# Optimization experiments

Measured on AMD Instinct MI355X. Metric: run time of the kernel, lower is better.

## Reference

```python
import jax, jax.numpy as jnp
import numpy as np

D_MODEL = 512
N_HEADS = 8
D_K = D_MODEL // N_HEADS
WINDOW = 32  # attention restricted to |i-j| <= WINDOW//2
SCALE = float(np.sqrt(D_K))


def setup_inputs() -> dict:
    key = jax.random.key(0)
    ks = jax.random.split(key, 11)
    B, S, D = 2, 4096, D_MODEL
    inv = 1.0 / np.sqrt(D)
    inp = {
        "query": jax.random.normal(ks[0], (B, S, D), jnp.float32),
        "key": jax.random.normal(ks[1], (B, S, D), jnp.float32),
        "value": jax.random.normal(ks[2], (B, S, D), jnp.float32),
        # torch nn.Linear params: weight (out,in), bias (out,)
        "wq": jax.random.uniform(ks[3], (D, D), jnp.float32, -inv, inv),
        "bq": jax.random.uniform(ks[4], (D,), jnp.float32, -inv, inv),
        "wk": jax.random.uniform(ks[5], (D, D), jnp.float32, -inv, inv),
        "bk": jax.random.uniform(ks[6], (D,), jnp.float32, -inv, inv),
        "wv": jax.random.uniform(ks[7], (D, D), jnp.float32, -inv, inv),
        "bv": jax.random.uniform(ks[8], (D,), jnp.float32, -inv, inv),
        "wo": jax.random.uniform(ks[9], (D, D), jnp.float32, -inv, inv),
        "bo": jax.random.uniform(ks[10], (D,), jnp.float32, -inv, inv),
    }
    return inp


def _linear(x, w, b):
    # torch: y = x @ w.T + b
    return jnp.einsum('bsd,od->bso', x, w) + b


def reference(query, key, value, wq, bq, wk, bk, wv, bv, wo, bo):
    B, S, D = query.shape
    # project and split heads -> [B, H, S, d_k]
    def split(x):
        return x.reshape(B, S, N_HEADS, D_K).transpose(0, 2, 1, 3)
    Q = split(_linear(query, wq, bq))
    K = split(_linear(key, wk, bk))
    V = split(_linear(value, wv, bv))
    # full scores then banded mask (faithful to original dense-masked impl)
    scores = jnp.einsum('bhqd,bhkd->bhqk', Q, K) / SCALE
    i = jnp.arange(S)[:, None]
    j = jnp.arange(S)[None, :]
    band = jnp.abs(i - j) <= (WINDOW // 2)  # [S, S]
    scores = jnp.where(band[None, None, :, :], scores, -1e9)
    attn = jax.nn.softmax(scores, axis=-1)
    ctx = jnp.einsum('bhqk,bhkd->bhqd', attn, V)
    ctx = ctx.transpose(0, 2, 1, 3).reshape(B, S, D)
    return _linear(ctx, wo, bo)
```

## Files before the change

kernel.cpp:

```cpp
#include <hip/hip_runtime.h>
#include <hip/hip_bf16.h>

using u16 = unsigned short;
using u32 = unsigned int;

typedef float f32x4 __attribute__((ext_vector_type(4)));
typedef __bf16 bf16x8 __attribute__((ext_vector_type(8)));

constexpr int B_ = 2;
constexpr int S_ = 4096;
constexpr int D_ = 512;
constexpr int H_ = 8;
constexpr int DK_ = 64;
constexpr int M_ = B_ * S_;
constexpr int K_ = 512;

__device__ __forceinline__ float bf2f(u16 u) {
  return __uint_as_float(((u32)u) << 16);
}
__device__ __forceinline__ u16 f2bf(float x) {
  u32 u = __float_as_uint(x);
  u = (u + 0x7fffu + ((u >> 16) & 1u)) >> 16;
  return (u16)u;
}
__device__ __forceinline__ u32 pack2(float a, float b) {
  return (u32)f2bf(a) | ((u32)f2bf(b) << 16);
}
__device__ __forceinline__ u32 cvtpk(float a, float b) {
  u32 r;
  asm("v_cvt_pk_bf16_f32 %0, %1, %2" : "=v"(r) : "v"(a), "v"(b));
  return r;
}

__device__ __forceinline__ void gload16(const void* g, void* l) {
  __builtin_amdgcn_global_load_lds((const __attribute__((address_space(1))) void*)g,
                                   (__attribute__((address_space(3))) void*)l,
                                   16, 0, 0);
}

constexpr int NG_W = 4 * (262144 / 8);

__global__ __launch_bounds__(256) void convert_w(
    const float* __restrict__ wq, const float* __restrict__ wk,
    const float* __restrict__ wv, const float* __restrict__ wo,
    u16* __restrict__ wqb, u16* __restrict__ wkb, u16* __restrict__ wvb,
    u16* __restrict__ wob)
{
  const int g8 = blockIdx.x * 256 + threadIdx.x;
  if (g8 >= NG_W) return;
  const int t = g8 >> 15;
  const int r = g8 & 32767;
  const float* s = (t == 0) ? wq : (t == 1) ? wk : (t == 2) ? wv : wo;
  u16* d = (t == 0) ? wqb : (t == 1) ? wkb : (t == 2) ? wvb : wob;
  const size_t off = (size_t)r * 8;
  const float4 x = *(const float4*)(s + off);
  const float4 y = *(const float4*)(s + off + 4);
  uint4 o;
  o.x = pack2(x.x, x.y); o.y = pack2(x.z, x.w);
  o.z = pack2(y.x, y.y); o.w = pack2(y.z, y.w);
  *(uint4*)(d + off) = o;
}

template<int MODE>
__device__ __forceinline__ void gemm_qkv_body(const float* __restrict__ A,
                                              const u16* __restrict__ Wt,
                                              const float* __restrict__ bias,
                                              void* __restrict__ Cout,
                                              float* __restrict__ Asf,
                                              u16* __restrict__ Bs)
{
  const int tid  = threadIdx.x;
  const int lane = tid & 63;
  const int w    = tid >> 6;
  const int wm   = w >> 1;
  const int wn   = w & 1;
  const int m0   = blockIdx.x * 128;
  const int n0   = blockIdx.y * 128;
  const int qr   = lane & 15;
  const int g    = lane >> 4;

  const int r4 = lane >> 4;
  const int c4 = (lane & 15) * 4;
  const int colx0 = c4 ^ (r4 << 3);
  const int colx1 = colx0 ^ 32;
  const float* arow = A + (size_t)(m0 + w * 32 + r4) * K_;

  auto stage_A = [&](int t) {
    const float* base = arow + t * 64;
#pragma unroll
    for (int p = 0; p < 8; ++p)
      gload16(base + (size_t)(p * 4) * K_ + ((p & 1) ? colx1 : colx0),
              Asf + (w * 32 + p * 4) * 64);
  };

  const int swz8 = ((lane & 7) ^ (lane >> 3)) * 8;
  const u16* b0 = Wt + (size_t)(n0 + w * 32 + (lane >> 3)) * K_ + swz8;
  auto stage_B = [&](int t) {
#pragma unroll
    for (int p = 0; p < 4; ++p)
      gload16(b0 + t * 64 + (size_t)p * 8 * K_, &Bs[(w * 32 + p * 8) * 64]);
  };

  f32x4 acc[4][4] = {};

  stage_A(0);
  stage_B(0);

  const int ax5 = (qr & 7) << 5;
  const int ax4 = (qr & 7) << 4;
  const char* ab = (const char*)Asf + (wm * 64 + qr) * 256;
  const char* bb = (const char*)Bs + (wn * 64 + qr) * 128;

  union U8 { u32 u[4]; bf16x8 v; };

  constexpr int NT = K_ / 64;
#pragma unroll 1
  for (int t = 0; t < NT; ++t) {
    __syncthreads();

#pragma unroll
    for (int kk = 0; kk < 2; ++kk) {
      bf16x8 af[4], bfr[4];
#pragma unroll
      for (int i = 0; i < 4; ++i) {
        const char* p = ab + i * 4096 + ((g * 32 + kk * 128) ^ ax5);
        const f32x4 lo = *(const f32x4*)p;
        const f32x4 hi = *(const f32x4*)(p + 16);
        U8 u;
        u.u[0] = cvtpk(lo[0], lo[1]);
        u.u[1] = cvtpk(lo[2], lo[3]);
        u.u[2] = cvtpk(hi[0], hi[1]);
        u.u[3] = cvtpk(hi[2], hi[3]);
        af[i] = u.v;
      }
#pragma unroll
      for (int j = 0; j < 4; ++j)
        bfr[j] = *(const bf16x8*)(bb + j * 2048 + ((g * 16 + kk * 64) ^ ax4));
#pragma unroll
      for (int i = 0; i < 4; ++i)
#pragma unroll
        for (int j = 0; j < 4; ++j)
          acc[i][j] = __builtin_amdgcn_mfma_f32_16x16x32_bf16(af[i], bfr[j], acc[i][j], 0, 0, 0);
    }

    if (t + 1 < NT) {
      __syncthreads();
      stage_A(t + 1);
      stage_B(t + 1);
    }
  }

#pragma unroll
  for (int j = 0; j < 4; ++j) {
    const int col = n0 + wn * 64 + j * 16 + qr;
    const float bv = bias[col];
#pragma unroll
    for (int i = 0; i < 4; ++i) {
      const int rbase = m0 + wm * 64 + i * 16 + g * 4;
      if constexpr (MODE == 2) {
        const int bb2 = rbase >> 12;
        const int ss = rbase & (S_ - 1);
        const int hh = col >> 6;
        const int dd = col & (DK_ - 1);
        uint2 pk;
        pk.x = pack2(acc[i][j][0] + bv, acc[i][j][1] + bv);
        pk.y = pack2(acc[i][j][2] + bv, acc[i][j][3] + bv);
        *(uint2*)&((u16*)Cout)[((size_t)((bb2 * H_ + hh) * DK_ + dd)) * S_ + ss] = pk;
      } else {
#pragma unroll
        for (int r = 0; r < 4; ++r)
          ((u16*)Cout)[(size_t)(rbase + r) * D_ + col] = f2bf(acc[i][j][r] + bv);
      }
    }
  }
}

__global__ __launch_bounds__(256, 3) void gemm_qkv(
    const float* __restrict__ q, const float* __restrict__ k, const float* __restrict__ v,
    const u16* __restrict__ wqb, const u16* __restrict__ wkb, const u16* __restrict__ wvb,
    const float* __restrict__ bq, const float* __restrict__ bk, const float* __restrict__ bv,
    u16* __restrict__ Qo, u16* __restrict__ Ko, u16* __restrict__ Vo)
{
  __shared__ float Asf[128 * 64];
  __shared__ u16   Bs[128 * 64];
  if (blockIdx.z == 0)      gemm_qkv_body<0>(q, wqb, bq, Qo, Asf, Bs);
  else if (blockIdx.z == 1) gemm_qkv_body<0>(k, wkb, bk, Ko, Asf, Bs);
  else                      gemm_qkv_body<2>(v, wvb, bv, Vo, Asf, Bs);
}

__global__ __launch_bounds__(256, 2) void gemm_out(
    const u16* __restrict__ A, const u16* __restrict__ Wt,
    const float* __restrict__ bias, float* __restrict__ C)
{
  __shared__ u16 As[64 * 64];
  __shared__ u16 Bs[128 * 64];

  const int tid  = threadIdx.x;
  const int lane = tid & 63;
  const int w    = tid >> 6;
  const int wm   = w >> 1;
  const int wn   = w & 1;
  const int m0   = blockIdx.x * 64;
  const int n0   = blockIdx.y * 128;
  const int qr   = lane & 15;
  const int g    = lane >> 4;

  const int swz8 = ((lane & 7) ^ (lane >> 3)) * 8;
  const u16* a0 = A  + (size_t)(m0 + w * 16 + (lane >> 3)) * K_ + swz8;
  const u16* b0 = Wt + (size_t)(n0 + w * 32 + (lane >> 3)) * K_ + swz8;

  auto stage = [&](int t) {
#pragma unroll
    for (int p = 0; p < 2; ++p)
      gload16(a0 + t * 64 + (size_t)p * 8 * K_, &As[(w * 16 + p * 8) * 64]);
#pragma unroll
    for (int p = 0; p < 4; ++p)
      gload16(b0 + t * 64 + (size_t)p * 8 * K_, &Bs[(w * 32 + p * 8) * 64]);
  };

  f32x4 acc[2][4] = {};
  stage(0);

  const int ax = (qr & 7) << 4;
  const char* ab = (const char*)As + (wm * 32 + qr) * 128;
  const char* bb = (const char*)Bs + (wn * 64 + qr) * 128;

  constexpr int NT = K_ / 64;
#pragma unroll 1
  for (int t = 0; t < NT; ++t) {
    __syncthreads();
#pragma unroll
    for (int kk = 0; kk < 2; ++kk) {
      bf16x8 af[2], bfr[4];
#pragma unroll
      for (int i = 0; i < 2; ++i)
        af[i]  = *(const bf16x8*)(ab + i * 2048 + ((g * 16 + kk * 64) ^ ax));
#pragma unroll
      for (int j = 0; j < 4; ++j)
        bfr[j] = *(const bf16x8*)(bb + j * 2048 + ((g * 16 + kk * 64) ^ ax));
#pragma unroll
      for (int i = 0; i < 2; ++i)
#pragma unroll
        for (int j = 0; j < 4; ++j)
          acc[i][j] = __builtin_amdgcn_mfma_f32_16x16x32_bf16(af[i], bfr[j], acc[i][j], 0, 0, 0);
    }
    if (t + 1 < NT) {
      __syncthreads();
      stage(t + 1);
    }
  }

#pragma unroll
  for (int j = 0; j < 4; ++j) {
    const int col = n0 + wn * 64 + j * 16 + qr;
    const float bv = bias[col];
#pragma unroll
    for (int i = 0; i < 2; ++i) {
      const int rbase = m0 + wm * 32 + i * 16 + g * 4;
#pragma unroll
      for (int r = 0; r < 4; ++r)
        C[(size_t)(rbase + r) * D_ + col] = acc[i][j][r] + bv;
    }
  }
}

__global__ __launch_bounds__(256) void attn_band_mfma(
    const u16* __restrict__ Q, const u16* __restrict__ K,
    const u16* __restrict__ Vt, u16* __restrict__ Ctx)
{
  constexpr int LDP = 72;
  __shared__ u16 P_lds[4][16 * LDP];

  const int lane = threadIdx.x & 63;
  const int w    = threadIdx.x >> 6;
  const int wid  = blockIdx.x * 4 + w;
  const int q0   = (wid & 255) << 4;
  const int bh   = wid >> 8;
  const int bb   = bh >> 3;
  const int hh   = bh & (H_ - 1);

  u16* pl = &P_lds[w][0];
  const int qr = lane & 15;
  const int g  = lane >> 4;

  *(uint2*)&pl[qr * LDP + 48 + 4 * g] = make_uint2(0u, 0u);

  bf16x8 qf[2];
  {
    const u16* qp = Q + ((size_t)(bb * S_ + q0 + qr)) * D_ + hh * DK_ + 8 * g;
    qf[0] = *(const bf16x8*)qp;
    qf[1] = *(const bf16x8*)(qp + 32);
  }

  f32x4 sc[3];
#pragma unroll
  for (int t = 0; t < 3; ++t) {
    int j = q0 - 16 + 16 * t + qr;
    j = min(max(j, 0), S_ - 1);
    const u16* kp = K + ((size_t)(bb * S_ + j)) * D_ + hh * DK_ + 8 * g;
    const bf16x8 kf0 = *(const bf16x8*)kp;
    const bf16x8 kf1 = *(const bf16x8*)(kp + 32);
    f32x4 a = {};
    a = __builtin_amdgcn_mfma_f32_16x16x32_bf16(kf0, qf[0], a, 0, 0, 0);
    a = __builtin_amdgcn_mfma_f32_16x16x32_bf16(kf1, qf[1], a, 0, 0, 0);
    sc[t] = a;
  }

  float s[3][4];
  float mx = -INFINITY;
#pragma unroll
  for (int t = 0; t < 3; ++t)
#pragma unroll
    for (int r = 0; r < 4; ++r) {
      const int joff = 16 * t + 4 * g + r;
      const int j = q0 - 16 + joff;
      const bool ok = (joff >= qr) && (joff <= qr + 32) && (j >= 0) && (j < S_);
      const float v = ok ? sc[t][r] * 0.125f : -INFINITY;
      s[t][r] = v;
      mx = fmaxf(mx, v);
    }
  mx = fmaxf(mx, __shfl_xor(mx, 16));
  mx = fmaxf(mx, __shfl_xor(mx, 32));

  float p[3][4];
  float den = 0.f;
#pragma unroll
  for (int t = 0; t < 3; ++t)
#pragma unroll
    for (int r = 0; r < 4; ++r) {
      p[t][r] = __expf(s[t][r] - mx);
      den += p[t][r];
    }
  den += __shfl_xor(den, 16);
  den += __shfl_xor(den, 32);
  const float inv = 1.0f / den;

#pragma unroll
  for (int t = 0; t < 3; ++t) {
    uint2 pk;
    pk.x = pack2(p[t][0] * inv, p[t][1] * inv);
    pk.y = pack2(p[t][2] * inv, p[t][3] * inv);
    *(uint2*)&pl[qr * LDP + 16 * t + 4 * g] = pk;
  }

  f32x4 cacc[4] = {};
#pragma unroll
  for (int jc = 0; jc < 2; ++jc) {
    const bf16x8 pa = *(const bf16x8*)&pl[qr * LDP + 8 * g + 32 * jc];
#pragma unroll
    for (int nt = 0; nt < 4; ++nt) {
      int jj = q0 - 16 + 8 * g + 32 * jc;
      jj = min(max(jj, 0), S_ - 8);
      const u16* vp = Vt + ((size_t)bh * DK_ + 16 * nt + qr) * S_ + jj;
      const bf16x8 vf = *(const bf16x8*)vp;
      cacc[nt] = __builtin_amdgcn_mfma_f32_16x16x32_bf16(pa, vf, cacc[nt], 0, 0, 0);
    }
  }

#pragma unroll
  for (int nt = 0; nt < 4; ++nt)
#pragma unroll
    for (int r = 0; r < 4; ++r) {
      const int qq = 4 * g + r;
      const int dd = 16 * nt + qr;
      Ctx[((size_t)(bb * S_ + q0 + qq)) * D_ + hh * DK_ + dd] = f2bf(cacc[nt][r]);
    }
}

extern "C" void kernel_launch(void* const* d_in, const int* in_sizes, int n_in,
                              void* d_out, int out_size, void* d_ws, size_t ws_size,
                              hipStream_t stream)
{
  const float* query = (const float*)d_in[0];
  const float* key   = (const float*)d_in[1];
  const float* value = (const float*)d_in[2];
  const float* wq    = (const float*)d_in[3];
  const float* bq    = (const float*)d_in[4];
  const float* wk    = (const float*)d_in[5];
  const float* bk    = (const float*)d_in[6];
  const float* wv    = (const float*)d_in[7];
  const float* bv    = (const float*)d_in[8];
  const float* wo    = (const float*)d_in[9];
  const float* bo    = (const float*)d_in[10];

  const size_t seg = (size_t)M_ * D_;
  u16* Qw  = (u16*)d_ws;
  u16* Kw  = Qw + seg;
  u16* Vw  = Kw + seg;
  u16* Cw  = Vw + seg;
  u16* wqb = Cw + seg;
  u16* wkb = wqb + (size_t)D_ * D_;
  u16* wvb = wkb + (size_t)D_ * D_;
  u16* wob = wvb + (size_t)D_ * D_;

  dim3 blk(256);
  convert_w<<<dim3((NG_W + 255) / 256), blk, 0, stream>>>(
      wq, wk, wv, wo, wqb, wkb, wvb, wob);
  gemm_qkv<<<dim3(M_ / 128, D_ / 128, 3), blk, 0, stream>>>(
      query, key, value, wqb, wkb, wvb, bq, bk, bv, Qw, Kw, Vw);
  attn_band_mfma<<<dim3((B_ * H_ * S_) / 64), blk, 0, stream>>>(Qw, Kw, Vw, Cw);
  gemm_out<<<dim3(M_ / 64, D_ / 128), blk, 0, stream>>>(Cw, wob, bo, (float*)d_out);
}
```

Before: 56.88 us.

## Convert fp32 A tiles to bf16 in registers before LDS store in QKV GEMM

The QKV projection GEMM used to copy fp32 activation tiles straight into LDS and convert them to bf16 on every MFMA operand read. Now each thread loads the next fp32 tile into registers while the current tile is being computed, converts it once, and writes bf16 into a swizzled LDS buffer. This halves the A-tile LDS footprint and read traffic, drops the repeated conversions, and overlaps the global load with compute. The cost is more live registers for the prefetched float4 values, which could limit occupancy under the 3-blocks launch bound.

```diff
diff --git a/kernel.cpp b/kernel.cpp
--- a/kernel.cpp
+++ b/kernel.cpp
@@ -66,7 +66,7 @@
                                               const u16* __restrict__ Wt,
                                               const float* __restrict__ bias,
                                               void* __restrict__ Cout,
-                                              float* __restrict__ Asf,
+                                              u16* __restrict__ As,
                                               u16* __restrict__ Bs)
 {
   const int tid  = threadIdx.x;
@@ -79,18 +79,30 @@
   const int qr   = lane & 15;
   const int g    = lane >> 4;
 
-  const int r4 = lane >> 4;
-  const int c4 = (lane & 15) * 4;
-  const int colx0 = c4 ^ (r4 << 3);
-  const int colx1 = colx0 ^ 32;
-  const float* arow = A + (size_t)(m0 + w * 32 + r4) * K_;
-
-  auto stage_A = [&](int t) {
-    const float* base = arow + t * 64;
-#pragma unroll
-    for (int p = 0; p < 8; ++p)
-      gload16(base + (size_t)(p * 4) * K_ + ((p & 1) ? colx1 : colx0),
-              Asf + (w * 32 + p * 4) * 64);
+  const int sr8 = tid >> 3;
+  const int c8  = tid & 7;
+  const float* afp = A + (size_t)(m0 + sr8) * K_ + c8 * 8;
+  char* awr = (char*)As + sr8 * 128 + ((c8 ^ (sr8 & 7)) * 16);
+
+  float4 ax_[4], ay_[4];
+  auto a_issue = [&](int t) {
+#pragma unroll
+    for (int p = 0; p < 4; ++p) {
+      const float* s = afp + t * 64 + (size_t)(p * 32) * K_;
+      ax_[p] = *(const float4*)s;
+      ay_[p] = *(const float4*)(s + 4);
+    }
+  };
+  auto a_write = [&]() {
+#pragma unroll
+    for (int p = 0; p < 4; ++p) {
+      uint4 o;
+      o.x = cvtpk(ax_[p].x, ax_[p].y);
+      o.y = cvtpk(ax_[p].z, ax_[p].w);
+      o.z = cvtpk(ay_[p].x, ay_[p].y);
+      o.w = cvtpk(ay_[p].z, ay_[p].w);
+      *(uint4*)(awr + p * 32 * 128) = o;
+    }
   };
 
   const int swz8 = ((lane & 7) ^ (lane >> 3)) * 8;
@@ -103,39 +115,30 @@
 
   f32x4 acc[4][4] = {};
 
-  stage_A(0);
+  a_issue(0);
+  a_write();
   stage_B(0);
 
-  const int ax5 = (qr & 7) << 5;
-  const int ax4 = (qr & 7) << 4;
-  const char* ab = (const char*)Asf + (wm * 64 + qr) * 256;
+  const int axr = (qr & 7) << 4;
+  const char* ab = (const char*)As + (wm * 64 + qr) * 128;
   const char* bb = (const char*)Bs + (wn * 64 + qr) * 128;
-
-  union U8 { u32 u[4]; bf16x8 v; };
 
   constexpr int NT = K_ / 64;
 #pragma unroll 1
   for (int t = 0; t < NT; ++t) {
     __syncthreads();
 
+    if (t + 1 < NT) a_issue(t + 1);
+
 #pragma unroll
     for (int kk = 0; kk < 2; ++kk) {
       bf16x8 af[4], bfr[4];
 #pragma unroll
-      for (int i = 0; i < 4; ++i) {
-        const char* p = ab + i * 4096 + ((g * 32 + kk * 128) ^ ax5);
-        const f32x4 lo = *(const f32x4*)p;
-        const f32x4 hi = *(const f32x4*)(p + 16);
-        U8 u;
-        u.u[0] = cvtpk(lo[0], lo[1]);
-        u.u[1] = cvtpk(lo[2], lo[3]);
-        u.u[2] = cvtpk(hi[0], hi[1]);
-        u.u[3] = cvtpk(hi[2], hi[3]);
-        af[i] = u.v;
-      }
+      for (int i = 0; i < 4; ++i)
+        af[i]  = *(const bf16x8*)(ab + i * 2048 + ((g * 16 + kk * 64) ^ axr));
 #pragma unroll
       for (int j = 0; j < 4; ++j)
-        bfr[j] = *(const bf16x8*)(bb + j * 2048 + ((g * 16 + kk * 64) ^ ax4));
+        bfr[j] = *(const bf16x8*)(bb + j * 2048 + ((g * 16 + kk * 64) ^ axr));
 #pragma unroll
       for (int i = 0; i < 4; ++i)
 #pragma unroll
@@ -145,7 +148,7 @@
 
     if (t + 1 < NT) {
       __syncthreads();
-      stage_A(t + 1);
+      a_write();
       stage_B(t + 1);
     }
   }
@@ -181,11 +184,11 @@
     const float* __restrict__ bq, const float* __restrict__ bk, const float* __restrict__ bv,
     u16* __restrict__ Qo, u16* __restrict__ Ko, u16* __restrict__ Vo)
 {
-  __shared__ float Asf[128 * 64];
-  __shared__ u16   Bs[128 * 64];
-  if (blockIdx.z == 0)      gemm_qkv_body<0>(q, wqb, bq, Qo, Asf, Bs);
-  else if (blockIdx.z == 1) gemm_qkv_body<0>(k, wkb, bk, Ko, Asf, Bs);
-  else                      gemm_qkv_body<2>(v, wvb, bv, Vo, Asf, Bs);
+  __shared__ u16 As[128 * 64];
+  __shared__ u16 Bs[128 * 64];
+  if (blockIdx.z == 0)      gemm_qkv_body<0>(q, wqb, bq, Qo, As, Bs);
+  else if (blockIdx.z == 1) gemm_qkv_body<0>(k, wkb, bk, Ko, As, Bs);
+  else                      gemm_qkv_body<2>(v, wvb, bv, Vo, As, Bs);
 }
 
 __global__ __launch_bounds__(256, 2) void gemm_out(
```

New measurement: 55.03 us. 3.2% less time.
